# Kernel tuning notes

Hardware: AMD Instinct MI355X
Metric: run time of the kernel (lower is better)

The kernel has to match this reference:

```python
import jax, jax.numpy as jnp
import numpy as np
import math

B, S, E = 2, 2048, 1024
H, HD = 16, 64  # num_heads, head_size


def setup_inputs() -> dict:
    key = jax.random.key(0)
    ks = jax.random.split(key, 9)
    sc = 1.0 / math.sqrt(HD)
    return {
        "x": jax.random.normal(ks[0], (B, S, E), dtype=jnp.float32),
        "Wq_w": jax.random.normal(ks[1], (HD, HD), dtype=jnp.float32) * sc,
        "Wq_b": jax.random.normal(ks[2], (HD,), dtype=jnp.float32) * 0.02,
        "Wk_w": jax.random.normal(ks[3], (HD, HD), dtype=jnp.float32) * sc,
        "Wk_b": jax.random.normal(ks[4], (HD,), dtype=jnp.float32) * 0.02,
        "Wv_w": jax.random.normal(ks[5], (HD, HD), dtype=jnp.float32) * sc,
        "Wv_b": jax.random.normal(ks[6], (HD,), dtype=jnp.float32) * 0.02,
        "proj_w": jax.random.normal(ks[7], (E, E), dtype=jnp.float32) * (1.0 / math.sqrt(E)),
        "proj_b": jax.random.normal(ks[8], (E,), dtype=jnp.float32) * 0.02,
    }


def reference(x, Wq_w, Wq_b, Wk_w, Wk_b, Wv_w, Wv_b, proj_w, proj_b):
    b, s, _ = x.shape
    xh = x.reshape(b, s, H, HD)  # split heads; QKV linears act per-head (shared weights)
    # torch Linear: y = x @ W.T + b
    q = jnp.einsum('bshd,ed->bhse', xh, Wq_w) + Wq_b  # [B,H,S,HD]
    k = jnp.einsum('bshd,ed->bhse', xh, Wk_w) + Wk_b
    v = jnp.einsum('bshd,ed->bhse', xh, Wv_w) + Wv_b
    scores = jnp.einsum('bhqd,bhkd->bhqk', q, k) / math.sqrt(HD)
    causal = jnp.tril(jnp.ones((s, s), dtype=bool))
    scores = jnp.where(causal, scores, jnp.float32(-1e20))
    attn = jax.nn.softmax(scores, axis=-1)  # attn_dropout p=0 (eval)
    out = jnp.einsum('bhqk,bhkd->bqhd', attn, v).reshape(b, s, H * HD)
    out = out @ proj_w.T + proj_b  # resid_dropout p=0 (eval)
    return out
```

## Files before the change

kernel.cpp:

```cpp
#include <hip/hip_runtime.h>
#include <hip/hip_bf16.h>

#define B_ 2
#define S_ 2048
#define E_ 1024
#define H_ 16
#define HD_ 64
#define T_ (B_ * S_)

typedef short bf16x8 __attribute__((ext_vector_type(8)));
typedef short bf16x4 __attribute__((ext_vector_type(4)));
typedef float f32x4 __attribute__((ext_vector_type(4)));

__device__ __forceinline__ short f2bf(float f) {
  union { float f; unsigned u; } v;
  v.f = f;
  unsigned r = v.u + 0x7fffu + ((v.u >> 16) & 1u);
  return (short)(r >> 16);
}

__device__ __forceinline__ int vperm_key(int cc) {
  return (cc & ~31) | (((cc >> 2) & 1) << 4) | (((cc >> 3) & 3) << 2) | (cc & 3);
}

__global__ __launch_bounds__(256) void convert_w_kernel(const float* __restrict__ src,
                                                        short* __restrict__ dst) {
  int i = (blockIdx.x * 256 + threadIdx.x) * 4;
  float4 f = *(const float4*)(src + i);
  bf16x4 o;
  o[0] = f2bf(f.x); o[1] = f2bf(f.y); o[2] = f2bf(f.z); o[3] = f2bf(f.w);
  *(bf16x4*)(dst + i) = o;
}

__global__ __launch_bounds__(256) void qkv_kernel(
    const float* __restrict__ x,
    const float* __restrict__ wq, const float* __restrict__ bq,
    const float* __restrict__ wk, const float* __restrict__ bk,
    const float* __restrict__ wv, const float* __restrict__ bv,
    short* __restrict__ Q, short* __restrict__ K, short* __restrict__ V) {
  __shared__ short Xs[64][136];
  __shared__ short Ws[192][72];
  __shared__ short Qt[64][68], Kt[64][68], Vt[64][68];

  const int tid = threadIdx.x;
  const int bid = blockIdx.x;
  const int tb = bid >> 3, hg = bid & 7;
  const int s0 = (tb * 64) & (S_ - 1);
  const int bb = (tb * 64) >> 11;
  const int wave = tid >> 6, lane = tid & 63;
  const int lrow = lane & 15, quad = lane >> 4;

#pragma unroll
  for (int i = 0; i < 8; i++) {
    int c = tid + 256 * i;
    int row = c >> 5, col4 = c & 31;
    float4 f = *(const float4*)(x + ((long)(tb * 64 + row)) * E_ + hg * 128 + col4 * 4);
    bf16x4 o;
    o[0] = f2bf(f.x); o[1] = f2bf(f.y); o[2] = f2bf(f.z); o[3] = f2bf(f.w);
    *(bf16x4*)&Xs[row][col4 * 4] = o;
  }
#pragma unroll
  for (int m = 0; m < 3; m++) {
    const float* w = (m == 0) ? wq : (m == 1) ? wk : wv;
#pragma unroll
    for (int i = 0; i < 4; i++) {
      int c = tid + 256 * i;
      int row = m * 64 + (c >> 4), col = (c & 15) * 4;
      float4 f = *(const float4*)(w + (long)c * 4);
      bf16x4 o;
      o[0] = f2bf(f.x); o[1] = f2bf(f.y); o[2] = f2bf(f.z); o[3] = f2bf(f.w);
      *(bf16x4*)&Ws[row][col] = o;
    }
  }
  float bias[12];
#pragma unroll
  for (int nb = 0; nb < 12; nb++) {
    int sel = nb >> 2;
    int e = ((nb & 3) * 16) + lrow;
    bias[nb] = ((sel == 0) ? bq : (sel == 1) ? bk : bv)[e];
  }
  __syncthreads();

  bf16x8 bf0[12], bf1[12];
#pragma unroll
  for (int nb = 0; nb < 12; nb++) {
    bf0[nb] = *(bf16x8*)&Ws[nb * 16 + lrow][quad * 8];
    bf1[nb] = *(bf16x8*)&Ws[nb * 16 + lrow][32 + quad * 8];
  }

  for (int hl = 0; hl < 2; hl++) {
    const int h = hg * 2 + hl;
    bf16x8 a0 = *(bf16x8*)&Xs[wave * 16 + lrow][hl * 64 + quad * 8];
    bf16x8 a1 = *(bf16x8*)&Xs[wave * 16 + lrow][hl * 64 + 32 + quad * 8];
#pragma unroll
    for (int nb = 0; nb < 12; nb++) {
      f32x4 acc = {0.f, 0.f, 0.f, 0.f};
      acc = __builtin_amdgcn_mfma_f32_16x16x32_bf16(a0, bf0[nb], acc, 0, 0, 0);
      acc = __builtin_amdgcn_mfma_f32_16x16x32_bf16(a1, bf1[nb], acc, 0, 0, 0);
      const int sel = nb >> 2;
      const float scale = (sel == 0) ? 0.125f : 1.0f;
      short (*ct)[68] = (sel == 0) ? Qt : (sel == 1) ? Kt : Vt;
#pragma unroll
      for (int r = 0; r < 4; r++) {
        ct[wave * 16 + quad * 4 + r][(nb & 3) * 16 + lrow] =
            f2bf((acc[r] + bias[nb]) * scale);
      }
    }
    __syncthreads();

    const int bh = bb * H_ + h;
    short* Qg = Q + ((long)bh * S_ + s0) * HD_;
    short* Kg = K + ((long)bh * S_ + s0) * HD_;
    short* Vg = V + (long)bh * HD_ * S_;
#pragma unroll
    for (int i = 0; i < 2; i++) {
      int c = tid + 256 * i;
      int row = c >> 3, col = (c & 7) * 8;
      *(bf16x8*)(Qg + (long)row * HD_ + col) = *(bf16x8*)&Qt[row][col];
      *(bf16x8*)(Kg + (long)row * HD_ + col) = *(bf16x8*)&Kt[row][col];
      bf16x8 vv;
#pragma unroll
      for (int j = 0; j < 8; j++) {
        int cc = col + j;
        vv[j] = Vt[vperm_key(cc)][row];
      }
      *(bf16x8*)(Vg + (long)row * S_ + s0 + col) = vv;
    }
    __syncthreads();
  }
}

__global__ __launch_bounds__(256) void attn_kernel(
    const short* __restrict__ Q, const short* __restrict__ K,
    const short* __restrict__ Vt, short* __restrict__ O ) {
  __shared__ short Ks[2][64][72];
  __shared__ short Vs[2][64][72];

  const int tid = threadIdx.x;
  const int bid = blockIdx.x;
  const int bh = bid & 31;
  const int pr = bid >> 5;
  const int b = bh >> 4, h = bh & 15;
  const long base = ((long)bh) << 17;

  const int wave = tid >> 6, lane = tid & 63;
  const int lrow = lane & 15, quad = lane >> 4;
  const int r0 = tid >> 3, c0 = (tid & 7) * 8;

  const short* Kg = K + base + (long)r0 * HD_ + c0;
  const short* Vg = Vt + base + (long)r0 * S_ + c0;

  const int qts[2] = {pr, 31 - pr};

  bf16x8 kreg0, kreg1, vreg0, vreg1;
  auto LD = [&](int k0) {
    kreg0 = *(const bf16x8*)(Kg + (long)k0 * HD_);
    kreg1 = *(const bf16x8*)(Kg + (long)k0 * HD_ + 32 * HD_);
    vreg0 = *(const bf16x8*)(Vg + k0);
    vreg1 = *(const bf16x8*)(Vg + 32 * S_ + k0);
  };

  LD(0);
  int it = 0;
  for (int ph = 0; ph < 2; ph++) {
    const int qt = qts[ph];
    const int q0w = qt * 64 + wave * 16;
    const int qg = q0w + lrow;
    const short* qp = Q + base + (long)qg * HD_;
    bf16x8 qf0 = *(const bf16x8*)(qp + quad * 8);
    bf16x8 qf1 = *(const bf16x8*)(qp + 32 + quad * 8);

    f32x4 Oacc[4];
#pragma unroll
    for (int db = 0; db < 4; db++) Oacc[db] = f32x4{0.f, 0.f, 0.f, 0.f};
    float lsum = 0.f;

    const int nkt = qt + 1;
    for (int kt = 0; kt < nkt; kt++, it++) {
      const int buf = it & 1;
      *(bf16x8*)&Ks[buf][r0][c0] = kreg0;
      *(bf16x8*)&Ks[buf][r0 + 32][c0] = kreg1;
      *(bf16x8*)&Vs[buf][r0][c0] = vreg0;
      *(bf16x8*)&Vs[buf][r0 + 32][c0] = vreg1;
      __syncthreads();

      {
        int ktn = kt + 1;
        bool have = true;
        if (ktn == nkt) {
          if (ph == 0) ktn = 0; else have = false;
        }
        if (have) LD(ktn * 64);
      }

      f32x4 sc[4];
#pragma unroll
      for (int nb = 0; nb < 4; nb++) {
        bf16x8 ka0 = *(bf16x8*)&Ks[buf][nb * 16 + lrow][quad * 8];
        bf16x8 ka1 = *(bf16x8*)&Ks[buf][nb * 16 + lrow][32 + quad * 8];
        f32x4 acc = {0.f, 0.f, 0.f, 0.f};
        acc = __builtin_amdgcn_mfma_f32_16x16x32_bf16(ka0, qf0, acc, 0, 0, 0);
        acc = __builtin_amdgcn_mfma_f32_16x16x32_bf16(ka1, qf1, acc, 0, 0, 0);
        sc[nb] = acc;
      }

      if (kt == qt) {
        const int k0 = kt * 64;
#pragma unroll
        for (int nb = 0; nb < 4; nb++) {
          int kgl = k0 + nb * 16 + quad * 4;
#pragma unroll
          for (int r = 0; r < 4; r++)
            if (kgl + r > qg) sc[nb][r] = -1e30f;
        }
      }

      bf16x4 pf[4];
#pragma unroll
      for (int nb = 0; nb < 4; nb++) {
#pragma unroll
        for (int r = 0; r < 4; r++) {
          float p = __expf(sc[nb][r]);
          union { float f; unsigned u; } pu;
          pu.f = p;
          unsigned t = pu.u & 0xffff0000u;
          union { unsigned u; float f; } tu;
          tu.u = t;
          lsum += tu.f;
          pf[nb][r] = (short)(pu.u >> 16);
        }
      }

#pragma unroll
      for (int p2 = 0; p2 < 2; p2++) {
#pragma unroll
        for (int db = 0; db < 4; db++) {
          bf16x8 vv = *(bf16x8*)&Vs[buf][db * 16 + lrow][p2 * 32 + quad * 8];
          bf16x4 vlo = {vv[0], vv[1], vv[2], vv[3]};
          bf16x4 vhi = {vv[4], vv[5], vv[6], vv[7]};
          Oacc[db] = __builtin_amdgcn_mfma_f32_16x16x16bf16_1k(vlo, pf[2 * p2], Oacc[db], 0, 0, 0);
          Oacc[db] = __builtin_amdgcn_mfma_f32_16x16x16bf16_1k(vhi, pf[2 * p2 + 1], Oacc[db], 0, 0, 0);
        }
      }
    }

    lsum += __shfl_xor(lsum, 16);
    lsum += __shfl_xor(lsum, 32);
    const float invl = 1.f / lsum;
    const long token = (long)b * S_ + qg;
    short* obase = O + token * E_ + h * HD_;
#pragma unroll
    for (int db = 0; db < 4; db++) {
      bf16x4 o;
#pragma unroll
      for (int r = 0; r < 4; r++) o[r] = f2bf(Oacc[db][r] * invl);
      *(bf16x4*)(obase + db * 16 + quad * 4) = o;
    }
  }
}

__global__ __launch_bounds__(256) void proj_kernel(
    const short* __restrict__ A, const short* __restrict__ W,
    const float* __restrict__ bias, float* __restrict__ out) {
  __shared__ short As[128][40];
  __shared__ short Bs[128][40];
  const int tid = threadIdx.x;
  const int bid = blockIdx.x;
  const int m0 = (bid >> 3) * 128;
  const int n0 = (bid & 7) * 128;
  const int wave = tid >> 6, lane = tid & 63;
  const int wm = wave >> 1, wn = wave & 1;
  const int lrow = lane & 15, quad = lane >> 4;

  f32x4 acc[4][4];
#pragma unroll
  for (int i = 0; i < 4; i++)
#pragma unroll
    for (int j = 0; j < 4; j++) acc[i][j] = f32x4{0.f, 0.f, 0.f, 0.f};

  for (int k0 = 0; k0 < E_; k0 += 32) {
#pragma unroll
    for (int i = 0; i < 2; i++) {
      int c = tid + 256 * i;
      int row = c >> 2, col = (c & 3) * 8;
      *(bf16x8*)&As[row][col] =
          *(const bf16x8*)(A + (long)(m0 + row) * E_ + k0 + col);
      *(bf16x8*)&Bs[row][col] =
          *(const bf16x8*)(W + (long)(n0 + row) * E_ + k0 + col);
    }
    __syncthreads();

    bf16x8 af[4], bf[4];
#pragma unroll
    for (int i = 0; i < 4; i++)
      af[i] = *(bf16x8*)&As[wm * 64 + i * 16 + lrow][quad * 8];
#pragma unroll
    for (int j = 0; j < 4; j++)
      bf[j] = *(bf16x8*)&Bs[wn * 64 + j * 16 + lrow][quad * 8];
#pragma unroll
    for (int i = 0; i < 4; i++)
#pragma unroll
      for (int j = 0; j < 4; j++)
        acc[i][j] = __builtin_amdgcn_mfma_f32_16x16x32_bf16(af[i], bf[j], acc[i][j], 0, 0, 0);
    __syncthreads();
  }

#pragma unroll
  for (int j = 0; j < 4; j++) {
    int col = n0 + wn * 64 + j * 16 + lrow;
    float bv = bias[col];
#pragma unroll
    for (int i = 0; i < 4; i++) {
#pragma unroll
      for (int r = 0; r < 4; r++) {
        int row = m0 + wm * 64 + i * 16 + quad * 4 + r;
        out[(long)row * E_ + col] = acc[i][j][r] + bv;
      }
    }
  }
}

extern "C" void kernel_launch(void* const* d_in, const int* in_sizes, int n_in,
                              void* d_out, int out_size, void* d_ws, size_t ws_size,
                              hipStream_t stream) {
  const float* x  = (const float*)d_in[0];
  const float* wq = (const float*)d_in[1];
  const float* bq = (const float*)d_in[2];
  const float* wk = (const float*)d_in[3];
  const float* bk = (const float*)d_in[4];
  const float* wv = (const float*)d_in[5];
  const float* bv = (const float*)d_in[6];
  const float* pw = (const float*)d_in[7];
  const float* pb = (const float*)d_in[8];
  float* out = (float*)d_out;

  char* ws = (char*)d_ws;
  const size_t qkv_bytes = (size_t)B_ * H_ * S_ * HD_ * 2;
  short* Qb = (short*)(ws);
  short* Kb = (short*)(ws + qkv_bytes);
  short* Vb = (short*)(ws + 2 * qkv_bytes);
  short* AO = (short*)(ws + 3 * qkv_bytes);
  short* PW = (short*)(ws + 3 * qkv_bytes + (size_t)T_ * E_ * 2);

  convert_w_kernel<<<dim3((E_ * E_) / 1024), dim3(256), 0, stream>>>(pw, PW);
  qkv_kernel<<<dim3((T_ / 64) * 8), dim3(256), 0, stream>>>(x, wq, bq, wk, bk, wv, bv,
                                                            Qb, Kb, Vb);
  attn_kernel<<<dim3(16 * 32), dim3(256), 0, stream>>>(Qb, Kb, Vb, AO);
  proj_kernel<<<dim3((T_ / 128) * (E_ / 128)), dim3(256), 0, stream>>>(AO, PW, pb, out);
}
```

Before: 156.9 us.

## Split attention keys across wave pairs, fuse weight convert, retile projection GEMM

Folds the projection-weight bf16 conversion into the QKV kernel as extra blocks, removing one launch. Attention now uses 32-row query tiles, with the two wave pairs in a block each taking alternating key tiles and combining partial outputs through shared memory. This doubles the grid and adds exp2 with log2e folded into the Q scale plus packed bf16 rounding. The projection GEMM moves to 128x64 tiles with a double-buffered LDS register prefetch and one barrier per k-step. The cost is extra barriers and reduction traffic in attention, and idle wave pairs on uneven key-tile counts.

```diff
diff --git a/kernel.cpp b/kernel.cpp
--- a/kernel.cpp
+++ b/kernel.cpp
@@ -23,26 +23,26 @@
   return (cc & ~31) | (((cc >> 2) & 1) << 4) | (((cc >> 3) & 3) << 2) | (cc & 3);
 }
 
-__global__ __launch_bounds__(256) void convert_w_kernel(const float* __restrict__ src,
-                                                        short* __restrict__ dst) {
-  int i = (blockIdx.x * 256 + threadIdx.x) * 4;
-  float4 f = *(const float4*)(src + i);
-  bf16x4 o;
-  o[0] = f2bf(f.x); o[1] = f2bf(f.y); o[2] = f2bf(f.z); o[3] = f2bf(f.w);
-  *(bf16x4*)(dst + i) = o;
-}
-
-__global__ __launch_bounds__(256) void qkv_kernel(
+__global__ __launch_bounds__(256) void qkv_conv_kernel(
     const float* __restrict__ x,
     const float* __restrict__ wq, const float* __restrict__ bq,
     const float* __restrict__ wk, const float* __restrict__ bk,
     const float* __restrict__ wv, const float* __restrict__ bv,
-    short* __restrict__ Q, short* __restrict__ K, short* __restrict__ V) {
+    short* __restrict__ Q, short* __restrict__ K, short* __restrict__ V,
+    const float* __restrict__ pw, short* __restrict__ pwb) {
+  const int tid = threadIdx.x;
+  if (blockIdx.x >= 512) {
+    int i = ((blockIdx.x - 512) * 256 + tid) * 4;
+    float4 f = *(const float4*)(pw + i);
+    bf16x4 o;
+    o[0] = f2bf(f.x); o[1] = f2bf(f.y); o[2] = f2bf(f.z); o[3] = f2bf(f.w);
+    *(bf16x4*)(pwb + i) = o;
+    return;
+  }
   __shared__ short Xs[64][136];
   __shared__ short Ws[192][72];
   __shared__ short Qt[64][68], Kt[64][68], Vt[64][68];
 
-  const int tid = threadIdx.x;
   const int bid = blockIdx.x;
   const int tb = bid >> 3, hg = bid & 7;
   const int s0 = (tb * 64) & (S_ - 1);
@@ -88,6 +88,7 @@
     bf1[nb] = *(bf16x8*)&Ws[nb * 16 + lrow][32 + quad * 8];
   }
 
+  const float QSCALE = 0.125f * 1.44269504089f;
   for (int hl = 0; hl < 2; hl++) {
     const int h = hg * 2 + hl;
     bf16x8 a0 = *(bf16x8*)&Xs[wave * 16 + lrow][hl * 64 + quad * 8];
@@ -98,7 +99,7 @@
       acc = __builtin_amdgcn_mfma_f32_16x16x32_bf16(a0, bf0[nb], acc, 0, 0, 0);
       acc = __builtin_amdgcn_mfma_f32_16x16x32_bf16(a1, bf1[nb], acc, 0, 0, 0);
       const int sel = nb >> 2;
-      const float scale = (sel == 0) ? 0.125f : 1.0f;
+      const float scale = (sel == 0) ? QSCALE : 1.0f;
       short (*ct)[68] = (sel == 0) ? Qt : (sel == 1) ? Kt : Vt;
 #pragma unroll
       for (int r = 0; r < 4; r++) {
@@ -130,11 +131,13 @@
   }
 }
 
-__global__ __launch_bounds__(256) void attn_kernel(
+__global__ __launch_bounds__(256, 4) void attn_kernel(
     const short* __restrict__ Q, const short* __restrict__ K,
     const short* __restrict__ Vt, short* __restrict__ O ) {
-  __shared__ short Ks[2][64][72];
-  __shared__ short Vs[2][64][72];
+  __shared__ __align__(16) char RAW[2 * 64 * 72 * 2 * 2];
+  short (*Ks)[64][72] = (short (*)[64][72])RAW;
+  short (*Vs)[64][72] = (short (*)[64][72])(RAW + 2 * 64 * 72 * 2);
+  float (*Cb)[64][20] = (float (*)[64][20])RAW;
 
   const int tid = threadIdx.x;
   const int bid = blockIdx.x;
@@ -144,28 +147,36 @@
   const long base = ((long)bh) << 17;
 
   const int wave = tid >> 6, lane = tid & 63;
+  const int c = wave >> 1;
+  const int s = wave & 1;
   const int lrow = lane & 15, quad = lane >> 4;
-  const int r0 = tid >> 3, c0 = (tid & 7) * 8;
-
-  const short* Kg = K + base + (long)r0 * HD_ + c0;
-  const short* Vg = Vt + base + (long)r0 * S_ + c0;
-
-  const int qts[2] = {pr, 31 - pr};
-
-  bf16x8 kreg0, kreg1, vreg0, vreg1;
+
+  const int ct = tid & 127;
+  const int r0 = ct >> 1, chc = (ct & 1) * 32;
+  const short* Kg = K + base + (long)r0 * HD_ + chc;
+  const short* Vg = Vt + base + (long)r0 * S_ + chc;
+
+  bf16x8 kreg[4], vreg[4];
   auto LD = [&](int k0) {
-    kreg0 = *(const bf16x8*)(Kg + (long)k0 * HD_);
-    kreg1 = *(const bf16x8*)(Kg + (long)k0 * HD_ + 32 * HD_);
-    vreg0 = *(const bf16x8*)(Vg + k0);
-    vreg1 = *(const bf16x8*)(Vg + 32 * S_ + k0);
+#pragma unroll
+    for (int j = 0; j < 4; j++) {
+      kreg[j] = *(const bf16x8*)(Kg + (long)k0 * HD_ + 8 * j);
+      vreg[j] = *(const bf16x8*)(Vg + k0 + 8 * j);
+    }
   };
 
-  LD(0);
-  int it = 0;
+  const int qts[2] = {pr, 63 - pr};
+  LD(c * 64);
+  bool nextld = false;
+
   for (int ph = 0; ph < 2; ph++) {
     const int qt = qts[ph];
-    const int q0w = qt * 64 + wave * 16;
-    const int qg = q0w + lrow;
+    const int nkt = (qt >> 1) + 1;
+    const int nc = (nkt + 1 - c) >> 1;
+    const int nit = (nkt + 1) >> 1;
+    if (ph == 1 && !nextld) LD(c * 64);
+
+    const int qg = qt * 32 + s * 16 + lrow;
     const short* qp = Q + base + (long)qg * HD_;
     bf16x8 qf0 = *(const bf16x8*)(qp + quad * 8);
     bf16x8 qf1 = *(const bf16x8*)(qp + 32 + quad * 8);
@@ -175,139 +186,169 @@
     for (int db = 0; db < 4; db++) Oacc[db] = f32x4{0.f, 0.f, 0.f, 0.f};
     float lsum = 0.f;
 
-    const int nkt = qt + 1;
-    for (int kt = 0; kt < nkt; kt++, it++) {
-      const int buf = it & 1;
-      *(bf16x8*)&Ks[buf][r0][c0] = kreg0;
-      *(bf16x8*)&Ks[buf][r0 + 32][c0] = kreg1;
-      *(bf16x8*)&Vs[buf][r0][c0] = vreg0;
-      *(bf16x8*)&Vs[buf][r0 + 32][c0] = vreg1;
+    for (int i = 0; i < nit; i++) {
+      const bool act = i < nc;
+      const int kt = 2 * i + c;
+      if (act) {
+#pragma unroll
+        for (int j = 0; j < 4; j++) {
+          *(bf16x8*)&Ks[c][r0][chc + 8 * j] = kreg[j];
+          *(bf16x8*)&Vs[c][r0][chc + 8 * j] = vreg[j];
+        }
+      }
       __syncthreads();
-
-      {
-        int ktn = kt + 1;
-        bool have = true;
-        if (ktn == nkt) {
-          if (ph == 0) ktn = 0; else have = false;
-        }
-        if (have) LD(ktn * 64);
-      }
-
-      f32x4 sc[4];
-#pragma unroll
-      for (int nb = 0; nb < 4; nb++) {
-        bf16x8 ka0 = *(bf16x8*)&Ks[buf][nb * 16 + lrow][quad * 8];
-        bf16x8 ka1 = *(bf16x8*)&Ks[buf][nb * 16 + lrow][32 + quad * 8];
-        f32x4 acc = {0.f, 0.f, 0.f, 0.f};
-        acc = __builtin_amdgcn_mfma_f32_16x16x32_bf16(ka0, qf0, acc, 0, 0, 0);
-        acc = __builtin_amdgcn_mfma_f32_16x16x32_bf16(ka1, qf1, acc, 0, 0, 0);
-        sc[nb] = acc;
-      }
-
-      if (kt == qt) {
-        const int k0 = kt * 64;
+      if (i + 1 < nc) {
+        LD((2 * (i + 1) + c) * 64);
+      } else if (ph == 0 && i + 1 == nc) {
+        LD(c * 64);
+        nextld = true;
+      }
+
+      if (act) {
+        f32x4 sc[4];
 #pragma unroll
         for (int nb = 0; nb < 4; nb++) {
-          int kgl = k0 + nb * 16 + quad * 4;
-#pragma unroll
-          for (int r = 0; r < 4; r++)
-            if (kgl + r > qg) sc[nb][r] = -1e30f;
-        }
-      }
-
-      bf16x4 pf[4];
-#pragma unroll
-      for (int nb = 0; nb < 4; nb++) {
-#pragma unroll
-        for (int r = 0; r < 4; r++) {
-          float p = __expf(sc[nb][r]);
-          union { float f; unsigned u; } pu;
-          pu.f = p;
-          unsigned t = pu.u & 0xffff0000u;
-          union { unsigned u; float f; } tu;
-          tu.u = t;
-          lsum += tu.f;
-          pf[nb][r] = (short)(pu.u >> 16);
-        }
-      }
-
-#pragma unroll
-      for (int p2 = 0; p2 < 2; p2++) {
-#pragma unroll
-        for (int db = 0; db < 4; db++) {
-          bf16x8 vv = *(bf16x8*)&Vs[buf][db * 16 + lrow][p2 * 32 + quad * 8];
-          bf16x4 vlo = {vv[0], vv[1], vv[2], vv[3]};
-          bf16x4 vhi = {vv[4], vv[5], vv[6], vv[7]};
-          Oacc[db] = __builtin_amdgcn_mfma_f32_16x16x16bf16_1k(vlo, pf[2 * p2], Oacc[db], 0, 0, 0);
-          Oacc[db] = __builtin_amdgcn_mfma_f32_16x16x16bf16_1k(vhi, pf[2 * p2 + 1], Oacc[db], 0, 0, 0);
-        }
-      }
-    }
-
-    lsum += __shfl_xor(lsum, 16);
-    lsum += __shfl_xor(lsum, 32);
-    const float invl = 1.f / lsum;
-    const long token = (long)b * S_ + qg;
-    short* obase = O + token * E_ + h * HD_;
-#pragma unroll
-    for (int db = 0; db < 4; db++) {
-      bf16x4 o;
-#pragma unroll
-      for (int r = 0; r < 4; r++) o[r] = f2bf(Oacc[db][r] * invl);
-      *(bf16x4*)(obase + db * 16 + quad * 4) = o;
-    }
+          bf16x8 ka0 = *(bf16x8*)&Ks[c][nb * 16 + lrow][quad * 8];
+          bf16x8 ka1 = *(bf16x8*)&Ks[c][nb * 16 + lrow][32 + quad * 8];
+          f32x4 acc = {0.f, 0.f, 0.f, 0.f};
+          acc = __builtin_amdgcn_mfma_f32_16x16x32_bf16(ka0, qf0, acc, 0, 0, 0);
+          acc = __builtin_amdgcn_mfma_f32_16x16x32_bf16(ka1, qf1, acc, 0, 0, 0);
+          sc[nb] = acc;
+        }
+
+        if (kt == nkt - 1) {
+          const int k0 = kt * 64;
+#pragma unroll
+          for (int nb = 0; nb < 4; nb++) {
+            int kgl = k0 + nb * 16 + quad * 4;
+#pragma unroll
+            for (int r = 0; r < 4; r++)
+              if (kgl + r > qg) sc[nb][r] = -1e30f;
+          }
+        }
+
+        bf16x4 pf[4];
+#pragma unroll
+        for (int nb = 0; nb < 4; nb++) {
+          unsigned u[4];
+#pragma unroll
+          for (int r = 0; r < 4; r++) {
+            float p = __builtin_amdgcn_exp2f(sc[nb][r]);
+            lsum += p;
+            u[r] = __float_as_uint(p) + 0x8000u;
+          }
+          unsigned lo = __builtin_amdgcn_perm(u[1], u[0], 0x07060302u);
+          unsigned hi = __builtin_amdgcn_perm(u[3], u[2], 0x07060302u);
+          union { unsigned q[2]; bf16x4 v; } pk;
+          pk.q[0] = lo; pk.q[1] = hi;
+          pf[nb] = pk.v;
+        }
+
+#pragma unroll
+        for (int p2 = 0; p2 < 2; p2++) {
+#pragma unroll
+          for (int db = 0; db < 4; db++) {
+            bf16x8 vv = *(bf16x8*)&Vs[c][db * 16 + lrow][p2 * 32 + quad * 8];
+            bf16x4 vlo = {vv[0], vv[1], vv[2], vv[3]};
+            bf16x4 vhi = {vv[4], vv[5], vv[6], vv[7]};
+            Oacc[db] = __builtin_amdgcn_mfma_f32_16x16x16bf16_1k(vlo, pf[2 * p2], Oacc[db], 0, 0, 0);
+            Oacc[db] = __builtin_amdgcn_mfma_f32_16x16x16bf16_1k(vhi, pf[2 * p2 + 1], Oacc[db], 0, 0, 0);
+          }
+        }
+      }
+      __syncthreads();
+    }
+
+    if (c == 1) {
+#pragma unroll
+      for (int db = 0; db < 4; db++) {
+        float4 o4 = make_float4(Oacc[db][0], Oacc[db][1], Oacc[db][2], Oacc[db][3]);
+        *(float4*)&Cb[s][lane][db * 4] = o4;
+      }
+      Cb[s][lane][16] = lsum;
+    }
+    __syncthreads();
+    if (c == 0) {
+#pragma unroll
+      for (int db = 0; db < 4; db++) {
+        float4 o4 = *(float4*)&Cb[s][lane][db * 4];
+        Oacc[db][0] += o4.x; Oacc[db][1] += o4.y;
+        Oacc[db][2] += o4.z; Oacc[db][3] += o4.w;
+      }
+      lsum += Cb[s][lane][16];
+      lsum += __shfl_xor(lsum, 16);
+      lsum += __shfl_xor(lsum, 32);
+      const float invl = 1.f / lsum;
+      const long token = (long)b * S_ + qg;
+      short* obase = O + token * E_ + h * HD_;
+#pragma unroll
+      for (int db = 0; db < 4; db++) {
+        bf16x4 o;
+#pragma unroll
+        for (int r = 0; r < 4; r++) o[r] = f2bf(Oacc[db][r] * invl);
+        *(bf16x4*)(obase + db * 16 + quad * 4) = o;
+      }
+    }
+    __syncthreads();
   }
 }
 
 __global__ __launch_bounds__(256) void proj_kernel(
     const short* __restrict__ A, const short* __restrict__ W,
     const float* __restrict__ bias, float* __restrict__ out) {
-  __shared__ short As[128][40];
-  __shared__ short Bs[128][40];
+  __shared__ short As[2][128][40];
+  __shared__ short Bs[2][64][40];
   const int tid = threadIdx.x;
   const int bid = blockIdx.x;
-  const int m0 = (bid >> 3) * 128;
-  const int n0 = (bid & 7) * 128;
+  const int m0 = (bid >> 4) * 128;
+  const int n0 = (bid & 15) * 64;
   const int wave = tid >> 6, lane = tid & 63;
   const int wm = wave >> 1, wn = wave & 1;
   const int lrow = lane & 15, quad = lane >> 4;
 
-  f32x4 acc[4][4];
+  const int ar = tid >> 1, ac = (tid & 1) * 16;
+  const int br = tid >> 2, bc = (tid & 3) * 8;
+
+  bf16x8 a0, a1, b0;
+  auto LDR = [&](int k0) {
+    const short* ap = A + (long)(m0 + ar) * E_ + k0 + ac;
+    a0 = *(const bf16x8*)(ap);
+    a1 = *(const bf16x8*)(ap + 8);
+    b0 = *(const bf16x8*)(W + (long)(n0 + br) * E_ + k0 + bc);
+  };
+
+  f32x4 acc[4][2];
 #pragma unroll
   for (int i = 0; i < 4; i++)
 #pragma unroll
-    for (int j = 0; j < 4; j++) acc[i][j] = f32x4{0.f, 0.f, 0.f, 0.f};
-
-  for (int k0 = 0; k0 < E_; k0 += 32) {
-#pragma unroll
-    for (int i = 0; i < 2; i++) {
-      int c = tid + 256 * i;
-      int row = c >> 2, col = (c & 3) * 8;
-      *(bf16x8*)&As[row][col] =
-          *(const bf16x8*)(A + (long)(m0 + row) * E_ + k0 + col);
-      *(bf16x8*)&Bs[row][col] =
-          *(const bf16x8*)(W + (long)(n0 + row) * E_ + k0 + col);
-    }
-    __syncthreads();
-
-    bf16x8 af[4], bf[4];
+    for (int j = 0; j < 2; j++) acc[i][j] = f32x4{0.f, 0.f, 0.f, 0.f};
+
+  LDR(0);
+  for (int kk = 0; kk < 32; kk++) {
+    const int buf = kk & 1;
+    *(bf16x8*)&As[buf][ar][ac] = a0;
+    *(bf16x8*)&As[buf][ar][ac + 8] = a1;
+    *(bf16x8*)&Bs[buf][br][bc] = b0;
+    __syncthreads();
+    if (kk < 31) LDR((kk + 1) * 32);
+
+    bf16x8 af[4], bfr[2];
 #pragma unroll
     for (int i = 0; i < 4; i++)
-      af[i] = *(bf16x8*)&As[wm * 64 + i * 16 + lrow][quad * 8];
-#pragma unroll
-    for (int j = 0; j < 4; j++)
-      bf[j] = *(bf16x8*)&Bs[wn * 64 + j * 16 + lrow][quad * 8];
+      af[i] = *(bf16x8*)&As[buf][wm * 64 + i * 16 + lrow][quad * 8];
+#pragma unroll
+    for (int j = 0; j < 2; j++)
+      bfr[j] = *(bf16x8*)&Bs[buf][wn * 32 + j * 16 + lrow][quad * 8];
 #pragma unroll
     for (int i = 0; i < 4; i++)
 #pragma unroll
-      for (int j = 0; j < 4; j++)
-        acc[i][j] = __builtin_amdgcn_mfma_f32_16x16x32_bf16(af[i], bf[j], acc[i][j], 0, 0, 0);
-    __syncthreads();
-  }
-
-#pragma unroll
-  for (int j = 0; j < 4; j++) {
-    int col = n0 + wn * 64 + j * 16 + lrow;
+      for (int j = 0; j < 2; j++)
+        acc[i][j] = __builtin_amdgcn_mfma_f32_16x16x32_bf16(af[i], bfr[j], acc[i][j], 0, 0, 0);
+  }
+
+#pragma unroll
+  for (int j = 0; j < 2; j++) {
+    int col = n0 + wn * 32 + j * 16 + lrow;
     float bv = bias[col];
 #pragma unroll
     for (int i = 0; i < 4; i++) {
@@ -342,9 +383,8 @@
   short* AO = (short*)(ws + 3 * qkv_bytes);
   short* PW = (short*)(ws + 3 * qkv_bytes + (size_t)T_ * E_ * 2);
 
-  convert_w_kernel<<<dim3((E_ * E_) / 1024), dim3(256), 0, stream>>>(pw, PW);
-  qkv_kernel<<<dim3((T_ / 64) * 8), dim3(256), 0, stream>>>(x, wq, bq, wk, bk, wv, bv,
-                                                            Qb, Kb, Vb);
-  attn_kernel<<<dim3(16 * 32), dim3(256), 0, stream>>>(Qb, Kb, Vb, AO);
-  proj_kernel<<<dim3((T_ / 128) * (E_ / 128)), dim3(256), 0, stream>>>(AO, PW, pb, out);
-}
+  qkv_conv_kernel<<<dim3(512 + 1024), dim3(256), 0, stream>>>(
+      x, wq, bq, wk, bk, wv, bv, Qb, Kb, Vb, pw, PW);
+  attn_kernel<<<dim3(32 * 32), dim3(256), 0, stream>>>(Qb, Kb, Vb, AO);
+  proj_kernel<<<dim3(32 * 16), dim3(256), 0, stream>>>(AO, PW, pb, out);
+}
```

Result: no change. 157.8 us (+0.6%).
